# Performance work log

Hardware: AMD Instinct MI355X
Metric: run time of the kernel (lower is better)

## Reference

```python
import jax, jax.numpy as jnp
import numpy as np

K = 20          # hard-coded self.k
NEG_SLOPE = 0.01


def _conv_bn_act(x, W, g, b):
    """1x1 conv (W: [Cout,Cin]) + eval-mode BN folded into per-channel g,b + LeakyReLU.
    x: (B, Cin, ...) -> (B, Cout, ...)"""
    y = jnp.einsum('oc,bc...->bo...', W, x)
    shp = (1, -1) + (1,) * (y.ndim - 2)
    return jax.nn.leaky_relu(y * g.reshape(shp) + b.reshape(shp), NEG_SLOPE)


def _knn_idx(x, k):
    """x: (B, C, N) -> idx (B, N, k) of k nearest neighbors (incl. self)."""
    xx = jnp.sum(x * x, axis=1)                      # (B, N)
    inner = jnp.einsum('bcn,bcm->bnm', x, x)         # (B, N, N)
    pair = 2.0 * inner - xx[:, :, None] - xx[:, None, :]  # -||xi-xj||^2
    return jax.lax.top_k(pair, k)[1]


def _gather(xt, idx):
    """xt: (B, N, C), idx: (B, N, k) -> (B, N, k, C)"""
    b = jnp.arange(xt.shape[0])[:, None, None]
    return xt[b, idx]


def _forward(x, w1, g1, b1, w2, g2, b2, wdg1, gdg1, bdg1, wdg2, gdg2, bdg2,
             wsn1, gsn1, bsn1, wsn2, gsn2, bsn2, w3, g3, b3, w4, g4, b4, w5, g5, b5):
    x0 = jnp.transpose(x, (0, 2, 1))                 # (B, 3, N) == xInit3d (t3d=False)
    h = _conv_bn_act(x0, w1, g1, b1)                 # (B, 64, N)
    h = _conv_bn_act(h, w2, g2, b2)                  # (B, 64, N)

    # Dynamic-graph EdgeConv: knn on features, edge = [x_i, x_j - x_i]
    idx1 = _knn_idx(h, K)                            # (B, N, K)
    ht = jnp.transpose(h, (0, 2, 1))                 # (B, N, 64)
    nbr = _gather(ht, idx1)                          # (B, N, K, 64)
    ctr = ht[:, :, None, :]                          # (B, N, 1, 64)
    edge = jnp.concatenate([jnp.broadcast_to(ctr, nbr.shape), nbr - ctr], axis=-1)
    edge = jnp.transpose(edge, (0, 3, 1, 2))         # (B, 128, N, K)
    h = _conv_bn_act(edge, wdg1, gdg1, bdg1)         # (B, 64, N, K)
    h = _conv_bn_act(h, wdg2, gdg2, bdg2)
    h = jnp.max(h, axis=-1)                          # (B, 64, N)

    # Spatial-neighborhood conv: knn on 3D coords, gather features only (cat=False)
    idx2 = _knn_idx(x0, K)                           # (B, N, K)
    feat2 = _gather(jnp.transpose(h, (0, 2, 1)), idx2)   # (B, N, K, 64)
    feat2 = jnp.transpose(feat2, (0, 3, 1, 2))       # (B, 64, N, K)
    h = _conv_bn_act(feat2, wsn1, gsn1, bsn1)
    h = _conv_bn_act(h, wsn2, gsn2, bsn2)
    h = jnp.max(h, axis=-1)                          # (B, 64, N)

    h = _conv_bn_act(h, w3, g3, b3)                  # (B, 64, N)
    h = _conv_bn_act(h, w4, g4, b4)                  # (B, 128, N)
    h = _conv_bn_act(h, w5, g5, b5)                  # (B, 512, N)
    return h[..., None]                             # (B, 512, N, 1)


def setup_inputs() -> dict:
    key = jax.random.key(0)
    ks = jax.random.split(key, 32)
    B, N = 8, 4096
    emb = 512
    d = {"x": jax.random.normal(ks[0], (B, N, 3), dtype=jnp.float32)}
    layers = [("1", 64, 3), ("2", 64, 64), ("dg1", 64, 128), ("dg2", 64, 64),
              ("sn1", 64, 64), ("sn2", 64, 64), ("3", 64, 64), ("4", 128, 64), ("5", emb, 128)]
    i = 1
    for name, co, ci in layers:
        d["w" + name] = jax.random.normal(ks[i], (co, ci), dtype=jnp.float32) * (1.0 / np.sqrt(ci))
        d["g" + name] = 1.0 + 0.1 * jax.random.normal(ks[i + 1], (co,), dtype=jnp.float32)
        d["b" + name] = 0.1 * jax.random.normal(ks[i + 2], (co,), dtype=jnp.float32)
        i += 3
    return d


def reference(x, w1, g1, b1, w2, g2, b2, wdg1, gdg1, bdg1, wdg2, gdg2, bdg2,
              wsn1, gsn1, bsn1, wsn2, gsn2, bsn2, w3, g3, b3, w4, g4, b4, w5, g5, b5):
    return _forward(x, w1, g1, b1, w2, g2, b2, wdg1, gdg1, bdg1, wdg2, gdg2, bdg2,
                    wsn1, gsn1, bsn1, wsn2, gsn2, bsn2, w3, g3, b3, w4, g4, b4, w5, g5, b5)
```

## Files before the change

### kernel.cpp

```cpp
#include <hip/hip_runtime.h>
#include <hip/hip_bf16.h>
#include <stdint.h>

typedef __hip_bfloat16 bf16;

#define N_   4096
#define NP   32768
#define KNN  20

#define OFF_H2   0L
#define OFF_XYZ  2097152L
#define OFF_X    2097152L
#define OFF_Y    2129920L
#define OFF_Z    2162688L
#define OFF_XX   2195456L
#define OFF_W2T  2195456L
#define OFF_XXC  2228224L
#define OFF_IDX1 2260992L
#define OFF_P4   2260992L
#define OFF_IDX2 2916352L
#define OFF_WF   3571712L
#define OFF_FLAG 3676480L
#define OFF_PAIR 3676544L
#define OFF_U    3676544L
#define OFF_V    5773696L
#define OFF_HDG  7870848L
#define OFF_H4   5773696L

#define WF_W1 0
#define WF_G1 192
#define WF_B1 256
#define WF_W2 320
#define WF_G2 4416
#define WF_B2 4480
#define WF_WDG1 4544
#define WF_GDG1 12736
#define WF_BDG1 12800
#define WF_WDG2 12864
#define WF_GDG2 16960
#define WF_BDG2 17024
#define WF_WSN1 17088
#define WF_GSN1 21184
#define WF_BSN1 21248
#define WF_WSN2 21312
#define WF_GSN2 25408
#define WF_BSN2 25472
#define WF_W3 25536
#define WF_G3 29632
#define WF_B3 29696
#define WF_W4 29760
#define WF_G4 37952
#define WF_B4 38080
#define WF_W5 38208
#define WF_G5 103744
#define WF_B5 104256
#define WF_END 104768

__device__ __forceinline__ float lrelu(float x){ return x >= 0.f ? x : 0.01f*x; }

__device__ __forceinline__ float distf(float xn,float yn,float zn,
                                       float xm,float ym,float zm,float cm){
  return fmaf(2.f, fmaf(xn,xm, fmaf(yn,ym, zn*zm)), -cm);
}

template<int CTRL>
__device__ __forceinline__ float fmax_dpp(float v){
  int o = __builtin_amdgcn_update_dpp(0, __float_as_int(v), CTRL, 0xF, 0xF, true);
  return fmaxf(v, __int_as_float(o));
}
__device__ __forceinline__ float wave_max_bcast(float v){
  v = fmax_dpp<0xB1>(v);
  v = fmax_dpp<0x4E>(v);
  v = fmax_dpp<0x124>(v);
  v = fmax_dpp<0x128>(v);
  v = fmax_dpp<0x142>(v);
  v = fmax_dpp<0x143>(v);
  return __int_as_float(__builtin_amdgcn_readlane(__float_as_int(v), 63));
}

__device__ __forceinline__ void ins2(float c, int m, float& k1, int& i1,
                                     float& k2, int& i2){
  bool g1 = c > k1, g2 = c > k2;
  k2 = g2 ? (g1 ? k1 : c) : k2;
  i2 = g2 ? (g1 ? i1 : m) : i2;
  k1 = g1 ? c : k1;
  i1 = g1 ? m : i1;
}

template<int MODE, typename F>
__device__ __forceinline__ void topk_pairs(float k1, int i1, float k2, int i2,
                                           int lane, F&& refetch,
                                           int* __restrict__ outp){
  const float NEGINF = -__builtin_inff();
  uint32_t mlo = 0, mhi = 0;
  int keep = 0;
  #pragma unroll 1
  for (int tt = 0; tt < KNN; tt++){
    float g = wave_max_bcast(k1);
    uint64_t ball = __ballot(k1 == g);
    int js = __builtin_amdgcn_readfirstlane((int)(__ffsll((unsigned long long)ball) - 1));
    int wid = __builtin_amdgcn_readlane(i1, js);
    int kown = __builtin_amdgcn_readlane(__float_as_int(k2), js);
    if (lane == tt) keep = wid;
    bool own = (lane == js);
    uint32_t ord = (MODE == 0) ? ((uint32_t)wid >> 6)
                               : ((((uint32_t)wid >> 8) << 2) | ((uint32_t)wid & 3u));
    uint32_t blo = (ord < 32u) ? (1u << ord) : 0u;
    uint32_t bhi = (ord >= 32u) ? (1u << (ord - 32u)) : 0u;
    mlo |= own ? blo : 0u;
    mhi |= own ? bhi : 0u;
    k1 = own ? k2 : k1;  i1 = own ? i2 : i1;
    k2 = own ? NEGINF : k2;
    if (kown == (int)0xFF800000u){
      uint32_t mre = (MODE == 0)
        ? ((uint32_t)js + ((uint32_t)lane << 6))
        : ((((uint32_t)lane >> 2) << 8) | (((uint32_t)js) << 2) | ((uint32_t)lane & 3u));
      float v = refetch(mre);
      uint32_t bl = (uint32_t)__builtin_amdgcn_readlane((int)mlo, js);
      uint32_t bh = (uint32_t)__builtin_amdgcn_readlane((int)mhi, js);
      uint64_t bm = ((uint64_t)bh << 32) | bl;
      if ((bm >> lane) & 1ull) v = NEGINF;
      float g2 = wave_max_bcast(v);
      uint64_t b2 = __ballot(v == g2);
      int jw = (int)(__ffsll((unsigned long long)b2) - 1);
      uint32_t wm = (MODE == 0)
        ? ((uint32_t)js + ((uint32_t)jw << 6))
        : ((((uint32_t)jw >> 2) << 8) | (((uint32_t)js) << 2) | ((uint32_t)jw & 3u));
      if (lane == js){ k1 = g2; i1 = (int)wm; }
    }
  }
  if (lane < KNN) outp[lane] = keep;
}

__global__ void k_detect(const void* __restrict__ x, int* __restrict__ flag){
  int lane = threadIdx.x;
  const bf16* xb = (const bf16*)x;
  int cnt = 0;
  #pragma unroll 1
  for (int i = lane; i < 256; i += 64){
    float v = __bfloat162float(xb[2*i]);
    float a = fabsf(v);
    if (a > 1e-3f && a < 100.f) cnt++;
  }
  #pragma unroll
  for (int off = 32; off; off >>= 1) cnt += __shfl_down(cnt, off, 64);
  if (lane == 0) *flag = (cnt >= 128) ? 0 : 1;
}

struct WPack {
  const void* p[27];
  int off[28];
};

__global__ void k_wcvt(WPack pk, float* __restrict__ dst, const int* __restrict__ flagp){
  int i = blockIdx.x*256 + threadIdx.x;
  if (i >= WF_END) return;
  int f = *flagp;
  #pragma unroll 1
  for (int s = 0; s < 27; s++){
    if (i < pk.off[s+1]){
      int j = i - pk.off[s];
      dst[i] = f ? ((const float*)pk.p[s])[j]
                 : __bfloat162float(((const bf16*)pk.p[s])[j]);
      return;
    }
  }
}

__global__ void k_wt(float* __restrict__ ws){
  const float* wf = ws + OFF_WF;
  int src = blockIdx.x ? WF_WSN2 : WF_WDG2;
  long dst = OFF_W2T + (long)blockIdx.x*4096;
  int t = threadIdx.x;
  #pragma unroll
  for (int i=t;i<4096;i+=256){
    int o = i >> 6, kk = i & 63;
    ws[dst + (long)kk*64 + o] = wf[src + o*64 + kk];
  }
}

__global__ void k_point(const void* __restrict__ x, float* __restrict__ ws){
  const float* wf = ws + OFF_WF;
  int f = ((const int*)(ws + OFF_FLAG))[0];
  int n = blockIdx.x*256 + threadIdx.x;
  float x0, x1, x2;
  if (f){
    const float* xf = (const float*)x;
    x0 = xf[n*3+0]; x1 = xf[n*3+1]; x2 = xf[n*3+2];
  } else {
    const bf16* xb = (const bf16*)x;
    x0 = __bfloat162float(xb[n*3+0]);
    x1 = __bfloat162float(xb[n*3+1]);
    x2 = __bfloat162float(xb[n*3+2]);
  }

  float h1[64];
  #pragma unroll
  for (int o=0;o<64;o++){
    float a = wf[WF_W1+o*3+0]*x0 + wf[WF_W1+o*3+1]*x1 + wf[WF_W1+o*3+2]*x2;
    h1[o] = lrelu(wf[WF_G1+o]*a + wf[WF_B1+o]);
  }
  float xx = 0.f;
  #pragma unroll 1
  for (int o=0;o<64;o++){
    float a = 0.f;
    #pragma unroll
    for (int c=0;c<64;c++) a += wf[WF_W2+o*64+c]*h1[c];
    float h2 = lrelu(wf[WF_G2+o]*a + wf[WF_B2+o]);
    ws[OFF_H2 + (long)n*64 + o] = h2;
    xx += h2*h2;
  }
  ws[OFF_XX + n] = xx;
  float cc = x0*x0 + x1*x1 + x2*x2;
  ws[OFF_X + n] = x0; ws[OFF_Y + n] = x1; ws[OFF_Z + n] = x2;
  ws[OFF_XXC + n] = cc;
  *(float4*)(ws + OFF_P4 + 4L*n) = make_float4(x0, x1, x2, cc);
}

__global__ __launch_bounds__(256) void k_pair(const float* __restrict__ ws, float* __restrict__ pair,
                                              int b, int n0){
  __shared__ float As[64*128];
  __shared__ float Bs[64*128];
  int t = threadIdx.x;
  int bx = blockIdx.x, by = blockIdx.y;
  const float* h2 = ws + OFF_H2 + (long)b*N_*64;

  int r = t >> 1, c0 = (t & 1)*32;
  const float4* arow = (const float4*)(h2 + (long)(n0 + by*128 + r)*64 + c0);
  const float4* brow = (const float4*)(h2 + (long)(bx*128 + r)*64 + c0);
  #pragma unroll
  for (int q=0;q<8;q++){
    float4 av = arow[q];
    As[(c0+4*q+0)*128 + r] = av.x; As[(c0+4*q+1)*128 + r] = av.y;
    As[(c0+4*q+2)*128 + r] = av.z; As[(c0+4*q+3)*128 + r] = av.w;
    float4 bv = brow[q];
    Bs[(c0+4*q+0)*128 + r] = bv.x; Bs[(c0+4*q+1)*128 + r] = bv.y;
    Bs[(c0+4*q+2)*128 + r] = bv.z; Bs[(c0+4*q+3)*128 + r] = bv.w;
  }
  __syncthreads();

  int tr = t/16, tc = t%16;
  float acc[8][8] = {};
  #pragma unroll 4
  for (int k=0;k<64;k++){
    const float4* ap = (const float4*)&As[k*128 + tr*8];
    const float4* bp = (const float4*)&Bs[k*128 + tc*8];
    float4 a0 = ap[0], a1 = ap[1], c0v = bp[0], c1v = bp[1];
    float a[8] = {a0.x,a0.y,a0.z,a0.w,a1.x,a1.y,a1.z,a1.w};
    float c[8] = {c0v.x,c0v.y,c0v.z,c0v.w,c1v.x,c1v.y,c1v.z,c1v.w};
    #pragma unroll
    for (int i=0;i<8;i++)
      #pragma unroll
      for (int j=0;j<8;j++) acc[i][j] += a[i]*c[j];
  }
  const float* xxp = ws + OFF_XX + b*N_ + bx*128 + tc*8;
  float xxm[8];
  #pragma unroll
  for (int j=0;j<8;j++) xxm[j] = xxp[j];
  #pragma unroll
  for (int i=0;i<8;i++){
    long row = (long)(by*128 + tr*8 + i)*N_ + bx*128 + tc*8;
    float4 o0 = make_float4(2.f*acc[i][0]-xxm[0], 2.f*acc[i][1]-xxm[1],
                            2.f*acc[i][2]-xxm[2], 2.f*acc[i][3]-xxm[3]);
    float4 o1 = make_float4(2.f*acc[i][4]-xxm[4], 2.f*acc[i][5]-xxm[5],
                            2.f*acc[i][6]-xxm[6], 2.f*acc[i][7]-xxm[7]);
    ((float4*)(pair+row))[0] = o0;
    ((float4*)(pair+row))[1] = o1;
  }
}

__global__ __launch_bounds__(256) void k_topk_pair(const float* __restrict__ pair, int* __restrict__ idx1,
                                                   int b, int n0){
  int t = threadIdx.x;
  int lane = t & 63, wv = t >> 6;
  int r = blockIdx.x*4 + wv;
  const float* rowp = pair + (long)r*N_;
  const float4* src = (const float4*)rowp;
  float k1 = -__builtin_inff(), k2 = -__builtin_inff();
  int i1 = 0, i2 = 0;
  #pragma unroll
  for (int q=0;q<16;q++){
    float4 v = src[lane + 64*q];
    int m0 = 4*lane + 256*q;
    ins2(v.x, m0,   k1,i1,k2,i2);
    ins2(v.y, m0+1, k1,i1,k2,i2);
    ins2(v.z, m0+2, k1,i1,k2,i2);
    ins2(v.w, m0+3, k1,i1,k2,i2);
  }
  topk_pairs<1>(k1,i1,k2,i2, lane, [&](uint32_t mre){ return rowp[mre]; },
                idx1 + (long)(b*N_ + n0 + r)*KNN);
}

__global__ __launch_bounds__(512) void k_knn2(const float* __restrict__ ws, int* __restrict__ idx2){
  __shared__ float4 pbuf[2][512];
  int t = threadIdx.x;
  int lane = t & 63, wv = t >> 6;
  int n = blockIdx.x*8 + wv;
  int base = n & ~4095;
  const float4* P4 = (const float4*)(ws + OFF_P4);
  float4 qp = P4[n];
  float xn = qp.x, yn = qp.y, zn = qp.z;
  float k1 = -__builtin_inff(), k2 = -__builtin_inff();
  int i1 = 0, i2 = 0;

  pbuf[0][t] = P4[base + t];
  __syncthreads();
  #pragma unroll 1
  for (int c = 0; c < 8; c++){
    float4 nx;
    if (c < 7) nx = P4[base + (c+1)*512 + t];
    const float4* pb = pbuf[c & 1];
    #pragma unroll
    for (int j = 0; j < 8; j++){
      float4 p = pb[lane + 64*j];
      int m = c*512 + 64*j + lane;
      ins2(distf(xn,yn,zn, p.x,p.y,p.z,p.w), m, k1,i1,k2,i2);
    }
    __syncthreads();
    if (c < 7) pbuf[(c+1) & 1][t] = nx;
    __syncthreads();
  }
  topk_pairs<0>(k1,i1,k2,i2, lane, [&](uint32_t mre){
      float4 p = P4[base + (int)mre];
      return distf(xn,yn,zn, p.x, p.y, p.z, p.w);
    }, idx2 + (long)n*KNN);
}

__global__ __launch_bounds__(256) void k_uv(float* __restrict__ ws){
  const float* wf = ws + OFF_WF;
  int t = threadIdx.x;
  int lane = t & 63;
  int W = blockIdx.x*4 + (t >> 6);
  int g = __builtin_amdgcn_readfirstlane(W >> 3);
  int s = __builtin_amdgcn_readfirstlane(W & 7);
  int n = g*64 + lane;
  int o0 = s*8;
  float h[64];
  const float4* src = (const float4*)(ws + OFF_H2 + (long)n*64);
  #pragma unroll
  for (int q=0;q<16;q++){ float4 v = src[q]; h[4*q]=v.x; h[4*q+1]=v.y; h[4*q+2]=v.z; h[4*q+3]=v.w; }
  float ua[8], vv[8];
  #pragma unroll 1
  for (int j=0;j<8;j++){
    int o = o0 + j;
    float va=0.f, vb=0.f;
    #pragma unroll
    for (int c=0;c<64;c++){
      va += wf[WF_WDG1+o*128+c]*h[c];
      vb += wf[WF_WDG1+o*128+64+c]*h[c];
    }
    ua[j] = va - vb;
    vv[j] = vb;
  }
  float* up = ws + OFF_U + (long)n*64 + o0;
  *(float4*)up     = make_float4(ua[0],ua[1],ua[2],ua[3]);
  *(float4*)(up+4) = make_float4(ua[4],ua[5],ua[6],ua[7]);
  float* vp = ws + OFF_V + (long)n*64 + o0;
  *(float4*)vp     = make_float4(vv[0],vv[1],vv[2],vv[3]);
  *(float4*)(vp+4) = make_float4(vv[4],vv[5],vv[6],vv[7]);
}

template<int USE_U>
__global__ __launch_bounds__(256) void k_edge(float* __restrict__ ws, const int* __restrict__ idxt,
      long uoff, long goff, long w2toff,
      int g1off, int b1off, int g2off, int b2off, long outoff){
  __shared__ float y1a[64*34];
  __shared__ float y1b[64*34];
  __shared__ int   idxs[32*KNN];
  const float* wf = ws + OFF_WF;
  const float4* w2t = (const float4*)(ws + w2toff);
  int t = threadIdx.x;
  int p0 = blockIdx.x*32;
  int b  = p0 >> 12;
  int lane = t & 63, wv = t >> 6;
  int tr = t & 15, oc = t >> 4;

  #pragma unroll 1
  for (int i=t;i<32*KNN;i+=256) idxs[i] = idxt[(long)p0*KNN + i];

  float ur[8];
  if (USE_U){
    #pragma unroll
    for (int jj=0;jj<8;jj++)
      ur[jj] = ws[uoff + (long)(p0 + wv*8 + jj)*64 + lane];
  } else {
    #pragma unroll
    for (int jj=0;jj<8;jj++) ur[jj] = 0.f;
  }
  float g1v = wf[g1off+lane], b1v = wf[b1off+lane];
  float g2r[4], b2r[4];
  #pragma unroll
  for (int j=0;j<4;j++){ g2r[j] = wf[g2off+oc*4+j]; b2r[j] = wf[b2off+oc*4+j]; }

  float mx[2][4];
  #pragma unroll
  for (int i=0;i<2;i++)
    #pragma unroll
    for (int j=0;j<4;j++) mx[i][j] = -3.0e38f;

  __syncthreads();

  long gbase = goff + ((long)b << 12)*64;
  float pfa[8], pfb[8];
  #pragma unroll
  for (int jj=0;jj<8;jj++){
    int e = wv*8 + jj;
    pfa[jj] = ws[gbase + (long)idxs[e*KNN + 0]*64 + lane];
    pfb[jj] = ws[gbase + (long)idxs[e*KNN + 1]*64 + lane];
  }

  for (int c=0;c<KNN/2;c++){
    #pragma unroll
    for (int jj=0;jj<8;jj++){
      int e = wv*8 + jj;
      float va = pfa[jj];
      float vb = pfb[jj];
      if (USE_U){ va += ur[jj]; vb += ur[jj]; }
      y1a[lane*34 + e] = lrelu(g1v*va + b1v);
      y1b[lane*34 + e] = lrelu(g1v*vb + b1v);
    }
    __syncthreads();
    if (c+1 < KNN/2){
      #pragma unroll
      for (int jj=0;jj<8;jj++){
        int e = wv*8 + jj;
        pfa[jj] = ws[gbase + (long)idxs[e*KNN + 2*c+2]*64 + lane];
        pfb[jj] = ws[gbase + (long)idxs[e*KNN + 2*c+3]*64 + lane];
      }
    }
    float acca[2][4] = {}, accb[2][4] = {};
    #pragma unroll 4
    for (int kk=0;kk<64;kk++){
      float2 a  = *(const float2*)&y1a[kk*34 + tr*2];
      float2 bb = *(const float2*)&y1b[kk*34 + tr*2];
      float4 cv = w2t[kk*16 + oc];
      float av[2] = {a.x, a.y};
      float bv[2] = {bb.x, bb.y};
      float cvv[4] = {cv.x, cv.y, cv.z, cv.w};
      #pragma unroll
      for (int i=0;i<2;i++)
        #pragma unroll
        for (int j=0;j<4;j++){
          acca[i][j] += av[i]*cvv[j];
          accb[i][j] += bv[i]*cvv[j];
        }
    }
    #pragma unroll
    for (int i=0;i<2;i++)
      #pragma unroll
      for (int j=0;j<4;j++){
        mx[i][j] = fmaxf(mx[i][j], lrelu(g2r[j]*acca[i][j] + b2r[j]));
        mx[i][j] = fmaxf(mx[i][j], lrelu(g2r[j]*accb[i][j] + b2r[j]));
      }
    __syncthreads();
  }
  #pragma unroll
  for (int i=0;i<2;i++)
    #pragma unroll
    for (int j=0;j<4;j++)
      ws[outoff + (long)(p0 + tr*2 + i)*64 + oc*4 + j] = mx[i][j];
}

__global__ __launch_bounds__(256) void k_w(float* __restrict__ ws){
  const float* wf = ws + OFF_WF;
  int t = threadIdx.x;
  int lane = t & 63;
  int W = blockIdx.x*4 + (t >> 6);
  int g = __builtin_amdgcn_readfirstlane(W >> 3);
  int s = __builtin_amdgcn_readfirstlane(W & 7);
  int n = g*64 + lane;
  int o0 = s*8;
  float h[64];
  const float4* src = (const float4*)(ws + OFF_HDG + (long)n*64);
  #pragma unroll
  for (int q=0;q<16;q++){ float4 v = src[q]; h[4*q]=v.x; h[4*q+1]=v.y; h[4*q+2]=v.z; h[4*q+3]=v.w; }
  float ua[8];
  #pragma unroll 1
  for (int j=0;j<8;j++){
    int o = o0 + j;
    float a = 0.f;
    #pragma unroll
    for (int c=0;c<64;c++) a += wf[WF_WSN1 + o*64 + c]*h[c];
    ua[j] = a;
  }
  float* up = ws + OFF_U + (long)n*64 + o0;
  *(float4*)up     = make_float4(ua[0],ua[1],ua[2],ua[3]);
  *(float4*)(up+4) = make_float4(ua[4],ua[5],ua[6],ua[7]);
}

__global__ __launch_bounds__(256) void k_h4(const float* __restrict__ ws, float* __restrict__ h4g){
  __shared__ float Hs[64*65];
  __shared__ float wb[64*130];
  const float* wf = ws + OFF_WF;
  int t = threadIdx.x;
  int p0 = blockIdx.x*64;

  {
    int r = t >> 2, c0 = (t & 3)*16;
    const float4* src = (const float4*)(ws + OFF_H2 + (long)(p0 + r)*64 + c0);
    #pragma unroll
    for (int q=0;q<4;q++){
      float4 v = src[q];
      Hs[(c0+4*q+0)*65 + r] = v.x; Hs[(c0+4*q+1)*65 + r] = v.y;
      Hs[(c0+4*q+2)*65 + r] = v.z; Hs[(c0+4*q+3)*65 + r] = v.w;
    }
  }
  {
    int r = t >> 2, c0 = (t & 3)*16;
    const float4* src = (const float4*)(wf + WF_W3 + (long)r*64 + c0);
    #pragma unroll
    for (int q=0;q<4;q++){
      float4 v = src[q];
      wb[(c0+4*q+0)*65 + r] = v.x; wb[(c0+4*q+1)*65 + r] = v.y;
      wb[(c0+4*q+2)*65 + r] = v.z; wb[(c0+4*q+3)*65 + r] = v.w;
    }
  }
  __syncthreads();

  int pr = t & 15, og = t >> 4;
  float acc[4][4] = {};
  #pragma unroll 8
  for (int k=0;k<64;k++){
    float4 a = *(const float4*)&Hs[k*65 + pr*4];
    float4 c = *(const float4*)&wb[k*65 + og*4];
    float av[4] = {a.x,a.y,a.z,a.w}, cv[4] = {c.x,c.y,c.z,c.w};
    #pragma unroll
    for (int i=0;i<4;i++)
      #pragma unroll
      for (int j=0;j<4;j++) acc[i][j] += av[i]*cv[j];
  }
  __syncthreads();

  #pragma unroll
  for (int j=0;j<4;j++){
    int o = og*4 + j;
    float g3 = wf[WF_G3+o], b3 = wf[WF_B3+o];
    #pragma unroll
    for (int i=0;i<4;i++)
      Hs[o*65 + pr*4 + i] = lrelu(g3*acc[i][j] + b3);
  }
  {
    int r = t >> 1, c0 = (t & 1)*32;
    const float4* src = (const float4*)(wf + WF_W4 + (long)r*64 + c0);
    #pragma unroll
    for (int q=0;q<8;q++){
      float4 v = src[q];
      wb[(c0+4*q+0)*130 + r] = v.x; wb[(c0+4*q+1)*130 + r] = v.y;
      wb[(c0+4*q+2)*130 + r] = v.z; wb[(c0+4*q+3)*130 + r] = v.w;
    }
  }
  __syncthreads();

  float a2[4][8] = {};
  #pragma unroll 8
  for (int k=0;k<64;k++){
    float4 a = *(const float4*)&Hs[k*65 + pr*4];
    float4 c0 = *(const float4*)&wb[k*130 + og*8];
    float4 c1 = *(const float4*)&wb[k*130 + og*8 + 4];
    float av[4] = {a.x,a.y,a.z,a.w};
    float cv[8] = {c0.x,c0.y,c0.z,c0.w,c1.x,c1.y,c1.z,c1.w};
    #pragma unroll
    for (int i=0;i<4;i++)
      #pragma unroll
      for (int j=0;j<8;j++) a2[i][j] += av[i]*cv[j];
  }
  #pragma unroll
  for (int j=0;j<8;j++){
    int o = og*8 + j;
    float g4 = wf[WF_G4+o], b4 = wf[WF_B4+o];
    #pragma unroll
    for (int i=0;i<4;i++)
      h4g[(long)o*NP + p0 + pr*4 + i] = lrelu(g4*a2[i][j] + b4);
  }
}

#define KC 32
__global__ __launch_bounds__(256) void k_conv5(const float* __restrict__ ws, void* __restrict__ outv){
  __shared__ float As[KC*128];
  __shared__ float Bs[KC*128];
  const float* wf = ws + OFF_WF;
  int f = ((const int*)(ws + OFF_FLAG))[0];
  int t = threadIdx.x;
  int p0 = blockIdx.x*128;
  int o0 = blockIdx.y*128;
  const float* H4 = ws + OFF_H4;
  float acc[8][8] = {};

  for (int kc = 0; kc < 128; kc += KC){
    {
      int r = t >> 1, c0 = (t & 1)*16;
      const float4* src = (const float4*)(wf + WF_W5 + (long)(o0 + r)*128 + kc + c0);
      #pragma unroll
      for (int q=0;q<4;q++){
        float4 v = src[q];
        As[(c0+4*q+0)*128 + r] = v.x; As[(c0+4*q+1)*128 + r] = v.y;
        As[(c0+4*q+2)*128 + r] = v.z; As[(c0+4*q+3)*128 + r] = v.w;
      }
    }
    {
      int kr = t >> 3, pc = (t & 7)*16;
      const float4* src = (const float4*)(H4 + (long)(kc + kr)*NP + p0 + pc);
      float4 v0 = src[0], v1 = src[1], v2 = src[2], v3 = src[3];
      *(float4*)&Bs[kr*128 + pc     ] = v0;
      *(float4*)&Bs[kr*128 + pc + 4 ] = v1;
      *(float4*)&Bs[kr*128 + pc + 8 ] = v2;
      *(float4*)&Bs[kr*128 + pc + 12] = v3;
    }
    __syncthreads();
    int tr = t/16, tc = t%16;
    #pragma unroll 8
    for (int k=0;k<KC;k++){
      const float4* ap = (const float4*)&As[k*128 + tr*8];
      const float4* bp = (const float4*)&Bs[k*128 + tc*8];
      float4 a0 = ap[0], a1 = ap[1], b0 = bp[0], b1 = bp[1];
      float a[8] = {a0.x,a0.y,a0.z,a0.w,a1.x,a1.y,a1.z,a1.w};
      float b[8] = {b0.x,b0.y,b0.z,b0.w,b1.x,b1.y,b1.z,b1.w};
      #pragma unroll
      for (int i=0;i<8;i++)
        #pragma unroll
        for (int j=0;j<8;j++) acc[i][j] += a[i]*b[j];
    }
    __syncthreads();
  }

  int tr = t/16, tc = t%16;
  int b = p0 >> 12, nn = (p0 & 4095) + tc*8;
  #pragma unroll
  for (int i=0;i<8;i++){
    int oo = o0 + tr*8 + i;
    float g5 = wf[WF_G5+oo], b5 = wf[WF_B5+oo];
    long base = ((long)(b*512 + oo) << 12) + nn;
    if (f){
      float4 v0 = make_float4(lrelu(g5*acc[i][0]+b5), lrelu(g5*acc[i][1]+b5),
                              lrelu(g5*acc[i][2]+b5), lrelu(g5*acc[i][3]+b5));
      float4 v1 = make_float4(lrelu(g5*acc[i][4]+b5), lrelu(g5*acc[i][5]+b5),
                              lrelu(g5*acc[i][6]+b5), lrelu(g5*acc[i][7]+b5));
      *(float4*)((float*)outv + base)     = v0;
      *(float4*)((float*)outv + base + 4) = v1;
    } else {
      #pragma unroll
      for (int j=0;j<8;j++)
        ((bf16*)outv)[base + j] = __float2bfloat16(lrelu(g5*acc[i][j] + b5));
    }
  }
}

extern "C" void kernel_launch(void* const* d_in, const int* in_sizes, int n_in,
                              void* d_out, int out_size, void* d_ws, size_t ws_size,
                              hipStream_t stream) {
  const void* X = d_in[0];
  float* ws = (float*)d_ws;
  int* flagp = (int*)(ws + OFF_FLAG);

  WPack pk;
  static const int wsz[27] = {192,64,64, 4096,64,64, 8192,64,64, 4096,64,64, 4096,64,64,
                              4096,64,64, 4096,64,64, 8192,128,128, 65536,512,512};
  int off = 0;
  for (int i=0;i<27;i++){ pk.p[i] = d_in[i+1]; pk.off[i] = off; off += wsz[i]; }
  pk.off[27] = off;

  k_detect<<<dim3(1), dim3(64), 0, stream>>>(X, flagp);
  k_wcvt<<<dim3((WF_END+255)/256), dim3(256), 0, stream>>>(pk, ws + OFF_WF, flagp);
  k_point<<<dim3(NP/256), dim3(256), 0, stream>>>(X, ws);
  k_knn2<<<dim3(NP/8), dim3(512), 0, stream>>>(ws, (int*)(ws + OFF_IDX2));

  long availf = (long)(ws_size/4) - OFF_PAIR;
  int chunk = 4096;
  if (availf < (long)N_*N_){
    long c = (availf / N_) & ~127L;
    chunk = (int)(c < 128 ? 128 : c);
    if (chunk > 4096) chunk = 4096;
  }
  for (int b=0;b<8;b++){
    for (int n0=0;n0<N_; n0+=chunk){
      int rows = (N_ - n0 < chunk) ? (N_ - n0) : chunk;
      k_pair<<<dim3(32, rows/128), dim3(256), 0, stream>>>(ws, ws + OFF_PAIR, b, n0);
      k_topk_pair<<<dim3(rows/4), dim3(256), 0, stream>>>(ws + OFF_PAIR, (int*)(ws + OFF_IDX1), b, n0);
    }
  }
  k_wt<<<dim3(2), dim3(256), 0, stream>>>(ws);
  k_uv<<<dim3(NP/32), dim3(256), 0, stream>>>(ws);
  k_edge<1><<<dim3(NP/32), dim3(256), 0, stream>>>(ws, (const int*)(ws + OFF_IDX1),
        OFF_U, OFF_V, OFF_W2T, WF_GDG1, WF_BDG1, WF_GDG2, WF_BDG2, OFF_HDG);
  k_w<<<dim3(NP/32), dim3(256), 0, stream>>>(ws);
  k_edge<0><<<dim3(NP/32), dim3(256), 0, stream>>>(ws, (const int*)(ws + OFF_IDX2),
        0, OFF_U, OFF_W2T + 4096, WF_GSN1, WF_BSN1, WF_GSN2, WF_BSN2, OFF_H2);
  k_h4<<<dim3(NP/64), dim3(256), 0, stream>>>(ws, ws + OFF_H4);
  k_conv5<<<dim3(NP/128, 4), dim3(256), 0, stream>>>(ws, d_out);
}
```

Measured before the change: 1.039 ms.

## Fuse feature-space pairwise distance GEMM with top-k selection in one kernel

Replaces the per-batch k_pair + k_topk_pair launches, which wrote a full 4096x4096 distance matrix to global memory and read it back, with a single fused kernel. Each block owns 64 query points, streams 128-candidate tiles of features through shared memory, computes the distance tile, and keeps running top-2 candidates per lane in registers. During the final top-k merge, distances are recomputed on demand from the features instead of being reread from a stored matrix. This removes the large global write/read and about 16 launches, but adds register pressure, more block-level syncs per tile, and recomputation during the merge.

```diff
diff --git a/kernel.cpp b/kernel.cpp
--- a/kernel.cpp
+++ b/kernel.cpp
@@ -21,7 +21,6 @@
 #define OFF_IDX2 2916352L
 #define OFF_WF   3571712L
 #define OFF_FLAG 3676480L
-#define OFF_PAIR 3676544L
 #define OFF_U    3676544L
 #define OFF_V    5773696L
 #define OFF_HDG  7870848L
@@ -217,78 +216,96 @@
   *(float4*)(ws + OFF_P4 + 4L*n) = make_float4(x0, x1, x2, cc);
 }
 
-__global__ __launch_bounds__(256) void k_pair(const float* __restrict__ ws, float* __restrict__ pair,
-                                              int b, int n0){
-  __shared__ float As[64*128];
-  __shared__ float Bs[64*128];
-  int t = threadIdx.x;
-  int bx = blockIdx.x, by = blockIdx.y;
-  const float* h2 = ws + OFF_H2 + (long)b*N_*64;
-
-  int r = t >> 1, c0 = (t & 1)*32;
-  const float4* arow = (const float4*)(h2 + (long)(n0 + by*128 + r)*64 + c0);
-  const float4* brow = (const float4*)(h2 + (long)(bx*128 + r)*64 + c0);
-  #pragma unroll
-  for (int q=0;q<8;q++){
-    float4 av = arow[q];
-    As[(c0+4*q+0)*128 + r] = av.x; As[(c0+4*q+1)*128 + r] = av.y;
-    As[(c0+4*q+2)*128 + r] = av.z; As[(c0+4*q+3)*128 + r] = av.w;
-    float4 bv = brow[q];
-    Bs[(c0+4*q+0)*128 + r] = bv.x; Bs[(c0+4*q+1)*128 + r] = bv.y;
-    Bs[(c0+4*q+2)*128 + r] = bv.z; Bs[(c0+4*q+3)*128 + r] = bv.w;
-  }
-  __syncthreads();
-
-  int tr = t/16, tc = t%16;
-  float acc[8][8] = {};
-  #pragma unroll 4
-  for (int k=0;k<64;k++){
-    const float4* ap = (const float4*)&As[k*128 + tr*8];
-    const float4* bp = (const float4*)&Bs[k*128 + tc*8];
-    float4 a0 = ap[0], a1 = ap[1], c0v = bp[0], c1v = bp[1];
-    float a[8] = {a0.x,a0.y,a0.z,a0.w,a1.x,a1.y,a1.z,a1.w};
-    float c[8] = {c0v.x,c0v.y,c0v.z,c0v.w,c1v.x,c1v.y,c1v.z,c1v.w};
-    #pragma unroll
-    for (int i=0;i<8;i++)
-      #pragma unroll
-      for (int j=0;j<8;j++) acc[i][j] += a[i]*c[j];
-  }
-  const float* xxp = ws + OFF_XX + b*N_ + bx*128 + tc*8;
-  float xxm[8];
-  #pragma unroll
-  for (int j=0;j<8;j++) xxm[j] = xxp[j];
-  #pragma unroll
-  for (int i=0;i<8;i++){
-    long row = (long)(by*128 + tr*8 + i)*N_ + bx*128 + tc*8;
-    float4 o0 = make_float4(2.f*acc[i][0]-xxm[0], 2.f*acc[i][1]-xxm[1],
-                            2.f*acc[i][2]-xxm[2], 2.f*acc[i][3]-xxm[3]);
-    float4 o1 = make_float4(2.f*acc[i][4]-xxm[4], 2.f*acc[i][5]-xxm[5],
-                            2.f*acc[i][6]-xxm[6], 2.f*acc[i][7]-xxm[7]);
-    ((float4*)(pair+row))[0] = o0;
-    ((float4*)(pair+row))[1] = o1;
-  }
-}
-
-__global__ __launch_bounds__(256) void k_topk_pair(const float* __restrict__ pair, int* __restrict__ idx1,
-                                                   int b, int n0){
-  int t = threadIdx.x;
+__global__ __launch_bounds__(256) void k_fknn(const float* __restrict__ ws, int* __restrict__ idx1){
+  __shared__ float As[64*64];
+  __shared__ float SB[64*128];
+  int t = threadIdx.x;
+  int p0 = blockIdx.x*64;
+  int base = p0 & ~4095;
+  const float* h2 = ws + OFF_H2;
+  const float* xxp = ws + OFF_XX + base;
   int lane = t & 63, wv = t >> 6;
-  int r = blockIdx.x*4 + wv;
-  const float* rowp = pair + (long)r*N_;
-  const float4* src = (const float4*)rowp;
-  float k1 = -__builtin_inff(), k2 = -__builtin_inff();
-  int i1 = 0, i2 = 0;
-  #pragma unroll
-  for (int q=0;q<16;q++){
-    float4 v = src[lane + 64*q];
-    int m0 = 4*lane + 256*q;
-    ins2(v.x, m0,   k1,i1,k2,i2);
-    ins2(v.y, m0+1, k1,i1,k2,i2);
-    ins2(v.z, m0+2, k1,i1,k2,i2);
-    ins2(v.w, m0+3, k1,i1,k2,i2);
-  }
-  topk_pairs<1>(k1,i1,k2,i2, lane, [&](uint32_t mre){ return rowp[mre]; },
-                idx1 + (long)(b*N_ + n0 + r)*KNN);
+  int tr = t & 15, tc = t >> 4;
+
+  {
+    int r = t >> 2, c0 = (t & 3)*16;
+    const float4* src = (const float4*)(h2 + (long)(p0 + r)*64 + c0);
+    #pragma unroll
+    for (int q=0;q<4;q++){
+      float4 v = src[q];
+      As[(c0+4*q+0)*64 + r] = v.x; As[(c0+4*q+1)*64 + r] = v.y;
+      As[(c0+4*q+2)*64 + r] = v.z; As[(c0+4*q+3)*64 + r] = v.w;
+    }
+  }
+
+  const float NEGINF = -__builtin_inff();
+  float k1a[16], k2a[16];
+  int i1a[16], i2a[16];
+  #pragma unroll
+  for (int rr=0;rr<16;rr++){ k1a[rr]=NEGINF; k2a[rr]=NEGINF; i1a[rr]=0; i2a[rr]=0; }
+
+  #pragma unroll 1
+  for (int tile=0; tile<32; tile++){
+    {
+      int c = t >> 1, c0 = (t & 1)*32;
+      const float4* src = (const float4*)(h2 + (long)(base + tile*128 + c)*64 + c0);
+      #pragma unroll
+      for (int q=0;q<8;q++){
+        float4 v = src[q];
+        SB[(c0+4*q+0)*128 + c] = v.x; SB[(c0+4*q+1)*128 + c] = v.y;
+        SB[(c0+4*q+2)*128 + c] = v.z; SB[(c0+4*q+3)*128 + c] = v.w;
+      }
+    }
+    __syncthreads();
+    float acc[4][8] = {};
+    #pragma unroll 4
+    for (int k=0;k<64;k++){
+      float4 a  = *(const float4*)&As[k*64 + tr*4];
+      float4 b0 = *(const float4*)&SB[k*128 + tc*8];
+      float4 b1 = *(const float4*)&SB[k*128 + tc*8 + 4];
+      float av[4] = {a.x,a.y,a.z,a.w};
+      float bv[8] = {b0.x,b0.y,b0.z,b0.w,b1.x,b1.y,b1.z,b1.w};
+      #pragma unroll
+      for (int i=0;i<4;i++)
+        #pragma unroll
+        for (int j=0;j<8;j++) acc[i][j] += av[i]*bv[j];
+    }
+    __syncthreads();
+    #pragma unroll
+    for (int i=0;i<4;i++){
+      *(float4*)&SB[(tr*4+i)*128 + tc*8]     = make_float4(acc[i][0],acc[i][1],acc[i][2],acc[i][3]);
+      *(float4*)&SB[(tr*4+i)*128 + tc*8 + 4] = make_float4(acc[i][4],acc[i][5],acc[i][6],acc[i][7]);
+    }
+    __syncthreads();
+    int m0 = tile*128 + lane;
+    float xx0 = xxp[m0], xx1 = xxp[m0 + 64];
+    #pragma unroll
+    for (int rr=0; rr<16; rr++){
+      int row = wv*16 + rr;
+      float d0 = 2.f*SB[row*128 + lane]      - xx0;
+      float d1 = 2.f*SB[row*128 + 64 + lane] - xx1;
+      ins2(d0, m0,      k1a[rr], i1a[rr], k2a[rr], i2a[rr]);
+      ins2(d1, m0 + 64, k1a[rr], i1a[rr], k2a[rr], i2a[rr]);
+    }
+    __syncthreads();
+  }
+
+  #pragma unroll 1
+  for (int rp=0; rp<16; rp++){
+    float k1v=NEGINF, k2v=NEGINF; int i1v=0, i2v=0;
+    #pragma unroll
+    for (int rr=0; rr<16; rr++)
+      if (rr == rp){ k1v=k1a[rr]; i1v=i1a[rr]; k2v=k2a[rr]; i2v=i2a[rr]; }
+    int n = p0 + wv*16 + rp;
+    const float* arow = h2 + (long)n*64;
+    topk_pairs<0>(k1v,i1v,k2v,i2v, lane, [&](uint32_t mre){
+        const float* crow = h2 + (long)(base + (int)mre)*64;
+        float d = 0.f;
+        #pragma unroll
+        for (int k=0;k<64;k++) d = fmaf(arow[k], crow[k], d);
+        return 2.f*d - xxp[mre];
+      }, idx1 + (long)n*KNN);
+  }
 }
 
 __global__ __launch_bounds__(512) void k_knn2(const float* __restrict__ ws, int* __restrict__ idx2){
@@ -663,21 +680,7 @@
   k_wcvt<<<dim3((WF_END+255)/256), dim3(256), 0, stream>>>(pk, ws + OFF_WF, flagp);
   k_point<<<dim3(NP/256), dim3(256), 0, stream>>>(X, ws);
   k_knn2<<<dim3(NP/8), dim3(512), 0, stream>>>(ws, (int*)(ws + OFF_IDX2));
-
-  long availf = (long)(ws_size/4) - OFF_PAIR;
-  int chunk = 4096;
-  if (availf < (long)N_*N_){
-    long c = (availf / N_) & ~127L;
-    chunk = (int)(c < 128 ? 128 : c);
-    if (chunk > 4096) chunk = 4096;
-  }
-  for (int b=0;b<8;b++){
-    for (int n0=0;n0<N_; n0+=chunk){
-      int rows = (N_ - n0 < chunk) ? (N_ - n0) : chunk;
-      k_pair<<<dim3(32, rows/128), dim3(256), 0, stream>>>(ws, ws + OFF_PAIR, b, n0);
-      k_topk_pair<<<dim3(rows/4), dim3(256), 0, stream>>>(ws + OFF_PAIR, (int*)(ws + OFF_IDX1), b, n0);
-    }
-  }
+  k_fknn<<<dim3(NP/64), dim3(256), 0, stream>>>(ws, (int*)(ws + OFF_IDX1));
   k_wt<<<dim3(2), dim3(256), 0, stream>>>(ws);
   k_uv<<<dim3(NP/32), dim3(256), 0, stream>>>(ws);
   k_edge<1><<<dim3(NP/32), dim3(256), 0, stream>>>(ws, (const int*)(ws + OFF_IDX1),
```

Result: slower. 1.574 ms (+51.4%).
